# Performance work log

Hardware: AMD Instinct MI355X
Metric: run time of the kernel (lower is better)

The kernel has to match this reference:

```python
import jax, jax.numpy as jnp
import numpy as np

B = 1024      # batch
HG = 28       # grid side (28x28 image -> graph)
N = HG * HG   # 784 nodes per sample
K = 70        # node_sampled (relaxed categorical classes)
GCN_OUT = 48
H_DIM = 400
Z = 70
IMG = 784
TEMP = 0.5


def _grid_edges():
    idx = np.arange(N).reshape(HG, HG)
    src = np.concatenate([idx[:, :-1].ravel(), idx[:, 1:].ravel(), idx[:-1, :].ravel(), idx[1:, :].ravel()])
    dst = np.concatenate([idx[:, 1:].ravel(), idx[:, :-1].ravel(), idx[1:, :].ravel(), idx[:-1, :].ravel()])
    loop = np.arange(N)
    return (np.concatenate([src, loop]).astype(np.int32),
            np.concatenate([dst, loop]).astype(np.int32))


def _lin(key, fi, fo):
    kw, kb = jax.random.split(key)
    s = 1.0 / np.sqrt(fi)
    return (jax.random.uniform(kw, (fi, fo), jnp.float32, -s, s),
            jax.random.uniform(kb, (fo,), jnp.float32, -s, s))


def setup_inputs() -> dict:
    key = jax.random.key(0)
    ks = jax.random.split(key, 16)
    src, dst = _grid_edges()
    u = jax.random.uniform(ks[2], (B, N, K), jnp.float32, 1e-6, 1.0 - 1e-6)
    inp = {
        'nodes': jax.random.normal(ks[0], (B, N, 2), jnp.float32),
        'logits': jax.random.normal(ks[1], (B, N, K), jnp.float32),
        'gumbel': -jnp.log(-jnp.log(u)),
        'eps': jax.random.normal(ks[3], (B, Z), jnp.float32),
    }
    inp['W1'], inp['b1'] = _lin(ks[4], 2, 16)
    inp['W2'], inp['b2'] = _lin(ks[5], 16, 32)
    inp['W3'], inp['b3'] = _lin(ks[6], 32, GCN_OUT)
    inp['We1'], inp['be1'] = _lin(ks[7], K * GCN_OUT, H_DIM)
    inp['We2'], inp['be2'] = _lin(ks[8], H_DIM, H_DIM)
    inp['Wmu'], inp['bmu'] = _lin(ks[9], H_DIM, Z)
    inp['Wvar'], inp['bvar'] = _lin(ks[10], H_DIM, Z)
    inp['Wd1'], inp['bd1'] = _lin(ks[11], Z, H_DIM)
    inp['Wd2'], inp['bd2'] = _lin(ks[12], H_DIM, IMG)
    inp['edge_src'] = jnp.asarray(src)
    inp['edge_dst'] = jnp.asarray(dst)
    return inp


def reference(nodes, logits, gumbel, eps,
              W1, b1, W2, b2, W3, b3,
              We1, be1, We2, be2,
              Wmu, bmu, Wvar, bvar,
              Wd1, bd1, Wd2, bd2,
              edge_src, edge_dst):
    # symmetric GCN normalization with self loops (already in edge list)
    deg = jnp.zeros((N,), nodes.dtype).at[edge_dst].add(1.0)
    dinv = jax.lax.rsqrt(deg)
    norm = dinv[edge_src] * dinv[edge_dst]  # [E]

    def gcn(h, W, b):
        h = h @ W                                   # [B,N,Fout]
        msg = h[:, edge_src] * norm[None, :, None]  # gather + scale, [B,E,Fout]
        return jnp.zeros_like(h).at[:, edge_dst].add(msg) + b

    h = jax.nn.relu(gcn(nodes, W1, b1))
    h = jax.nn.relu(gcn(h, W2, b2))
    h = jax.nn.relu(gcn(h, W3, b3))            # [B,N,48]

    # RelaxedOneHotCategorical(temp=0.5).rsample() == gumbel-softmax
    sample = jax.nn.softmax((logits + gumbel) / TEMP, axis=-1)  # [B,N,K]
    g = jnp.einsum('bnk,bnf->bkf', sample, h).reshape(h.shape[0], K * GCN_OUT)

    # encoder MLP + reparameterize
    e = jax.nn.relu(g @ We1 + be1)
    e = jax.nn.relu(e @ We2 + be2)
    mu = e @ Wmu + bmu
    var = jax.nn.softplus(e @ Wvar + bvar)
    z = mu + eps * jnp.sqrt(var + 1e-10)

    # decoder
    d = jax.nn.relu(z @ Wd1 + bd1)
    x_rec = jax.nn.sigmoid(d @ Wd2 + bd2)      # [B,784]
    return x_rec
```

## Files before the change

kernel.cpp:

```cpp
#include <hip/hip_runtime.h>
#include <hip/hip_bf16.h>


#define BB 1024
#define HG 28
#define NN 784
#define KK 70
#define F3 48
#define HD 400
#define ZD 70
#define IMGD 784

typedef __hip_bfloat16 bf16;
typedef __attribute__((ext_vector_type(8))) short s8v;
typedef __attribute__((ext_vector_type(4))) float f32x4;

__device__ __forceinline__ float dinv_ij(int i, int j){
  int deg = 1 + (i>0) + (i<HG-1) + (j>0) + (j<HG-1);
  return rsqrtf((float)deg);
}

__device__ __forceinline__ unsigned pk2(float a, float b){
  union { bf16 h; unsigned short u; } ua, ub;
  ua.h = __float2bfloat16(a); ub.h = __float2bfloat16(b);
  return ((unsigned)ub.u << 16) | ua.u;
}

__global__ __launch_bounds__(256, 2)
void gcn_fused(const float* __restrict__ nodes,
               const float* __restrict__ W1, const float* __restrict__ b1,
               const float* __restrict__ W2, const float* __restrict__ b2,
               const float* __restrict__ W3, const float* __restrict__ b3,
               bf16* __restrict__ h3){
  __shared__ __align__(16) char smem[73216];
  float* regA = (float*)smem;
  float* regB = (float*)(smem + 36288);
  float* wbuf = (float*)(smem + 64512);
  float* W1s = wbuf;          float* b1s = wbuf + 32;
  float* W2s = wbuf + 48;     float* b2s = wbuf + 560;
  float* W3s = wbuf + 592;    float* b3s = wbuf + 2128;

  int tid = threadIdx.x;
  if (tid < 32)  W1s[tid] = W1[tid];
  if (tid < 16)  b1s[tid] = b1[tid];
  for (int t = tid; t < 512;  t += 256) W2s[t] = W2[t];
  if (tid < 32)  b2s[tid] = b2[tid];
  for (int t = tid; t < 1536; t += 256) W3s[t] = W3[t];
  if (tid < 48)  b3s[tid] = b3[tid];

  int b = blockIdx.x >> 2, s = blockIdx.x & 3;
  int base3 = s*7;
  int base2 = base3 - 1;
  int base1 = base3 - 2;
  const float* nb = nodes + (size_t)b*NN*2;
  __syncthreads();

  {
    float* h1s = regA;
    for (int t = tid; t < 308; t += 256){
      int lr = t/28, j = t - lr*28;
      int r = base1 + lr;
      float o[16] __attribute__((aligned(16)));
      if (r < 0 || r >= HG){
        #pragma unroll
        for (int f=0; f<16; f++) o[f] = 0.f;
      } else {
        float dn = dinv_ij(r,j);
        float a0 = dn*nb[(r*HG+j)*2+0], a1 = dn*nb[(r*HG+j)*2+1];
        if (r > 0)   { float w=dinv_ij(r-1,j); a0 += w*nb[((r-1)*HG+j)*2]; a1 += w*nb[((r-1)*HG+j)*2+1]; }
        if (r < HG-1){ float w=dinv_ij(r+1,j); a0 += w*nb[((r+1)*HG+j)*2]; a1 += w*nb[((r+1)*HG+j)*2+1]; }
        if (j > 0)   { float w=dinv_ij(r,j-1); a0 += w*nb[(r*HG+j-1)*2];   a1 += w*nb[(r*HG+j-1)*2+1]; }
        if (j < HG-1){ float w=dinv_ij(r,j+1); a0 += w*nb[(r*HG+j+1)*2];   a1 += w*nb[(r*HG+j+1)*2+1]; }
        a0 *= dn; a1 *= dn;
        #pragma unroll
        for (int f=0; f<16; f++) o[f] = fmaxf(a0*W1s[f] + a1*W1s[16+f] + b1s[f], 0.f);
      }
      float* dst = h1s + t*20;
      #pragma unroll
      for (int q=0; q<4; q++) *(float4*)(dst + 4*q) = *(float4*)&o[4*q];
    }
  }
  __syncthreads();

  if (tid < 252){
    const float* h1s = regA;
    float* agg1 = regB;
    int lr = tid/28, j = tid - lr*28;
    int r = base2 + lr;
    float o[16] __attribute__((aligned(16)));
    if (r < 0 || r >= HG){
      #pragma unroll
      for (int f=0; f<16; f++) o[f] = 0.f;
    } else {
      int ln = (lr+1)*28 + j;
      float dn = dinv_ij(r,j);
      float wu = dinv_ij(r-1,j), wd = dinv_ij(r+1,j);
      float wl = (j>0)    ? dinv_ij(r,j-1) : 0.f;
      float wr = (j<HG-1) ? dinv_ij(r,j+1) : 0.f;
      const float* pc = h1s + ln*20;
      #pragma unroll
      for (int q=0; q<4; q++){
        float4 vc = *(const float4*)(pc + 4*q);
        float4 vu = *(const float4*)(pc - 28*20 + 4*q);
        float4 vd = *(const float4*)(pc + 28*20 + 4*q);
        float4 vl = *(const float4*)(pc - 20 + 4*q);
        float4 vr = *(const float4*)(pc + 20 + 4*q);
        o[4*q+0] = dn*(dn*vc.x + wu*vu.x + wd*vd.x + wl*vl.x + wr*vr.x);
        o[4*q+1] = dn*(dn*vc.y + wu*vu.y + wd*vd.y + wl*vl.y + wr*vr.y);
        o[4*q+2] = dn*(dn*vc.z + wu*vu.z + wd*vd.z + wl*vl.z + wr*vr.z);
        o[4*q+3] = dn*(dn*vc.w + wu*vu.w + wd*vd.w + wl*vl.w + wr*vr.w);
      }
    }
    float* dst = agg1 + tid*20;
    #pragma unroll
    for (int q=0; q<4; q++) *(float4*)(dst + 4*q) = *(float4*)&o[4*q];
  }
  __syncthreads();

  {
    const float* agg1 = regB;
    float* h2s = regA;
    int tx = tid & 7, ty = tid >> 3;
    float4 w2r[16];
    #pragma unroll
    for (int fi=0; fi<16; fi++) w2r[fi] = *(const float4*)&W2s[fi*32 + tx*4];
    float4 bb = *(const float4*)&b2s[tx*4];
    #pragma unroll
    for (int i=0; i<8; i++){
      int n = ty + 32*i;
      if (n < 252){
        float af[16] __attribute__((aligned(16)));
        const float* ap = agg1 + n*20;
        #pragma unroll
        for (int q=0; q<4; q++) *(float4*)&af[4*q] = *(const float4*)(ap + 4*q);
        float4 acc = bb;
        #pragma unroll
        for (int fi=0; fi<16; fi++){
          float a = af[fi];
          acc.x += a*w2r[fi].x; acc.y += a*w2r[fi].y;
          acc.z += a*w2r[fi].z; acc.w += a*w2r[fi].w;
        }
        acc.x = fmaxf(acc.x,0.f); acc.y = fmaxf(acc.y,0.f);
        acc.z = fmaxf(acc.z,0.f); acc.w = fmaxf(acc.w,0.f);
        *(float4*)&h2s[n*36 + tx*4] = acc;
      }
    }
  }
  __syncthreads();

  if (tid < 196){
    const float* h2s = regA;
    float* agg2 = regB;
    int lr = tid/28, j = tid - lr*28;
    int r = base3 + lr;
    int ln = (lr+1)*28 + j;
    float dn = dinv_ij(r,j);
    float wu = dinv_ij(r-1,j), wd = dinv_ij(r+1,j);
    float wl = (j>0)    ? dinv_ij(r,j-1) : 0.f;
    float wr = (j<HG-1) ? dinv_ij(r,j+1) : 0.f;
    const float* pc = h2s + ln*36;
    float* dst = agg2 + tid*36;
    #pragma unroll
    for (int q=0; q<8; q++){
      float4 vc = *(const float4*)(pc + 4*q);
      float4 vu = *(const float4*)(pc - 28*36 + 4*q);
      float4 vd = *(const float4*)(pc + 28*36 + 4*q);
      float4 vl = *(const float4*)(pc - 36 + 4*q);
      float4 vr = *(const float4*)(pc + 36 + 4*q);
      float4 o;
      o.x = dn*(dn*vc.x + wu*vu.x + wd*vd.x + wl*vl.x + wr*vr.x);
      o.y = dn*(dn*vc.y + wu*vu.y + wd*vd.y + wl*vl.y + wr*vr.y);
      o.z = dn*(dn*vc.z + wu*vu.z + wd*vd.z + wl*vl.z + wr*vr.z);
      o.w = dn*(dn*vc.w + wu*vu.w + wd*vd.w + wl*vl.w + wr*vr.w);
      *(float4*)(dst + 4*q) = o;
    }
  }
  __syncthreads();

  {
    bf16* h3buf = (bf16*)regA;
    if (tid < 252){
      const float* agg2 = regB;
      int tx = tid % 12, ty = tid / 12;
      float4 w3r[32];
      #pragma unroll
      for (int fi=0; fi<32; fi++) w3r[fi] = *(const float4*)&W3s[fi*48 + tx*4];
      float4 bb = *(const float4*)&b3s[tx*4];
      #pragma unroll
      for (int i=0; i<10; i++){
        int n = ty + 21*i;
        if (n < 196){
          float af[32] __attribute__((aligned(16)));
          const float* ap = agg2 + n*36;
          #pragma unroll
          for (int q=0; q<8; q++) *(float4*)&af[4*q] = *(const float4*)(ap + 4*q);
          float4 acc = bb;
          #pragma unroll
          for (int fi=0; fi<32; fi++){
            float a = af[fi];
            acc.x += a*w3r[fi].x; acc.y += a*w3r[fi].y;
            acc.z += a*w3r[fi].z; acc.w += a*w3r[fi].w;
          }
          uint2 pv;
          pv.x = pk2(fmaxf(acc.x,0.f), fmaxf(acc.y,0.f));
          pv.y = pk2(fmaxf(acc.z,0.f), fmaxf(acc.w,0.f));
          *(uint2*)((char*)h3buf + n*112 + tx*8) = pv;
        }
      }
    }
  }
  __syncthreads();

  {
    const char* h3buf = (const char*)regA;
    uint4* dst = (uint4*)(h3 + ((size_t)b*NN + base3*28)*F3);
    for (int t = tid; t < 1176; t += 256){
      int n = t/6, gq = t - n*6;
      dst[t] = *(const uint4*)(h3buf + n*112 + gq*16);
    }
  }
}

__global__ __launch_bounds__(256, 2)
void einsum_mfma_kernel(const float* __restrict__ logits, const float* __restrict__ gumbel,
                        const bf16* __restrict__ h3, float* __restrict__ g){
  __shared__ __align__(16) char smem[72256];
  float* samp = (float*)smem;
  short* stp  = (short*)smem;
  short* stlo = (short*)(smem + 21760);
  short* htp  = (short*)(smem + 43520);
  float* cred = (float*)(smem + 43520 + 13056);

  int b = blockIdx.x;
  int tid = threadIdx.x;
  int l = tid & 63, w = tid >> 6;

  f32x4 acc[5][3];
  #pragma unroll
  for (int mt=0; mt<5; mt++)
    #pragma unroll
    for (int bt=0; bt<3; bt++) acc[mt][bt] = (f32x4){0.f,0.f,0.f,0.f};

  for (int chunk = 0; chunk < 7; chunk++){
    int c0 = chunk*128;
    int nvalid = min(128, NN - c0);
    __syncthreads();

    {
      const float4* l4 = (const float4*)(logits + ((size_t)b*NN + c0)*KK);
      const float4* g4 = (const float4*)(gumbel + ((size_t)b*NN + c0)*KK);
      int lim = nvalid*KK/4;
      for (int t = tid; t < 2240; t += 256){
        if (t < lim){
          float4 lv = l4[t], gv = g4[t];
          float xs[4] = {2.f*(lv.x+gv.x), 2.f*(lv.y+gv.y), 2.f*(lv.z+gv.z), 2.f*(lv.w+gv.w)};
          int e = t*4;
          #pragma unroll
          for (int i2=0;i2<4;i2++){
            int n = (e+i2)/KK, k = (e+i2) - KK*n;
            samp[n*72 + k] = xs[i2];
          }
        }
      }
    }
    {
      int n = tid & 127, fh = tid >> 7;
      bool valid = n < nvalid;
      const uint2* src = (const uint2*)(h3 + ((size_t)b*NN + c0 + n)*F3 + fh*24);
      #pragma unroll
      for (int j=0; j<6; j++){
        uint2 v = valid ? src[j] : (uint2){0u,0u};
        int f0 = fh*24 + j*4;
        htp[(f0+0)*136 + n] = (short)(v.x & 0xFFFFu);
        htp[(f0+1)*136 + n] = (short)(v.x >> 16);
        htp[(f0+2)*136 + n] = (short)(v.y & 0xFFFFu);
        htp[(f0+3)*136 + n] = (short)(v.y >> 16);
      }
    }
    __syncthreads();

    int nl = tid >> 1, h = tid & 1;
    bool valid = nl < nvalid;
    float p[35];
    if (valid){
      float x[35], m = -1e30f;
      #pragma unroll
      for (int t=0; t<35; t++){ x[t] = samp[nl*72 + h*35 + t]; m = fmaxf(m, x[t]); }
      m = fmaxf(m, __shfl_xor(m, 1));
      float sum = 0.f;
      #pragma unroll
      for (int t=0; t<35; t++){ x[t] = __expf(x[t]-m); sum += x[t]; }
      sum += __shfl_xor(sum, 1);
      float r = 1.0f/sum;
      #pragma unroll
      for (int t=0; t<35; t++) p[t] = x[t]*r;
    } else {
      #pragma unroll
      for (int t=0; t<35; t++) p[t] = 0.f;
    }
    __syncthreads();

    #pragma unroll
    for (int t=0; t<35; t++){
      int k = h*35 + t;
      bf16 hi = __float2bfloat16(p[t]);
      float lo = p[t] - __bfloat162float(hi);
      *(bf16*)&stp[k*136 + nl]  = hi;
      *(bf16*)&stlo[k*136 + nl] = __float2bfloat16(lo);
    }
    __syncthreads();

    {
      int n0 = w*32 + (l>>4)*8;
      s8v bfr[3];
      #pragma unroll
      for (int bt=0; bt<3; bt++)
        bfr[bt] = *(const s8v*)&htp[(bt*16 + (l&15))*136 + n0];
      #pragma unroll
      for (int mt=0; mt<5; mt++){
        s8v ah = *(const s8v*)&stp[(mt*16 + (l&15))*136 + n0];
        s8v al = *(const s8v*)&stlo[(mt*16 + (l&15))*136 + n0];
        #pragma unroll
        for (int bt=0; bt<3; bt++){
          acc[mt][bt] = __builtin_amdgcn_mfma_f32_16x16x32_bf16(ah, bfr[bt], acc[mt][bt], 0, 0, 0);
          acc[mt][bt] = __builtin_amdgcn_mfma_f32_16x16x32_bf16(al, bfr[bt], acc[mt][bt], 0, 0, 0);
        }
      }
    }
  }

  __syncthreads();
  for (int rw = 0; rw < 4; rw++){
    if (w == rw){
      #pragma unroll
      for (int mt=0; mt<5; mt++)
        #pragma unroll
        for (int bt=0; bt<3; bt++)
          #pragma unroll
          for (int r=0; r<4; r++){
            int row = mt*16 + (l>>4)*4 + r;
            int col = bt*16 + (l&15);
            if (rw == 0) cred[row*49 + col] = acc[mt][bt][r];
            else         cred[row*49 + col] += acc[mt][bt][r];
          }
    }
    __syncthreads();
  }
  for (int t = tid; t < KK*F3; t += 256){
    int r = t / F3, c = t - r*F3;
    g[(size_t)b*(KK*F3) + t] = cred[r*49 + c];
  }
}

template<int ACT>
__global__ __launch_bounds__(256)
void dense_kernel(const float* __restrict__ A, const float* __restrict__ W,
                  const float* __restrict__ bias, float* __restrict__ out,
                  int M, int K, int Nn, int kChunk){
  __shared__ float As[16][65];
  __shared__ float Bs[16][64];
  int tx = threadIdx.x & 15, ty = threadIdx.x >> 4;
  int m0 = blockIdx.x*64, n0 = blockIdx.y*64;
  int ks = blockIdx.z * kChunk;
  int ke = min(K, ks + kChunk);
  int a_kk = threadIdx.x & 15, a_mm = threadIdx.x >> 4;
  int b_nn = threadIdx.x & 63, b_k0 = threadIdx.x >> 6;
  float ra[4], rb[4];
  float acc[4][4] = {};

  #pragma unroll
  for (int s=0; s<4; s++){
    int gk = ks + a_kk;
    ra[s] = (gk < ke) ? A[(size_t)(m0 + a_mm + s*16)*K + gk] : 0.f;
  }
  #pragma unroll
  for (int s=0; s<4; s++){
    int gk = ks + b_k0 + s*4, gn = n0 + b_nn;
    rb[s] = (gk < ke && gn < Nn) ? W[(size_t)gk*Nn + gn] : 0.f;
  }

  for (int k0 = ks; k0 < ke; k0 += 16){
    #pragma unroll
    for (int s=0; s<4; s++) As[a_kk][a_mm + s*16] = ra[s];
    #pragma unroll
    for (int s=0; s<4; s++) Bs[b_k0 + s*4][b_nn] = rb[s];
    __syncthreads();
    if (k0 + 16 < ke){
      #pragma unroll
      for (int s=0; s<4; s++){
        int gk = k0 + 16 + a_kk;
        ra[s] = (gk < ke) ? A[(size_t)(m0 + a_mm + s*16)*K + gk] : 0.f;
      }
      #pragma unroll
      for (int s=0; s<4; s++){
        int gk = k0 + 16 + b_k0 + s*4, gn = n0 + b_nn;
        rb[s] = (gk < ke && gn < Nn) ? W[(size_t)gk*Nn + gn] : 0.f;
      }
    }
    #pragma unroll
    for (int kk=0; kk<16; kk++){
      float a[4], bv[4];
      #pragma unroll
      for (int i2=0; i2<4; i2++) a[i2] = As[kk][ty*4+i2];
      #pragma unroll
      for (int j2=0; j2<4; j2++) bv[j2] = Bs[kk][tx*4+j2];
      #pragma unroll
      for (int i2=0; i2<4; i2++)
        #pragma unroll
        for (int j2=0; j2<4; j2++) acc[i2][j2] += a[i2]*bv[j2];
    }
    __syncthreads();
  }

  if (ACT == 2){
    float* po = out + (size_t)blockIdx.z*M*Nn;
    #pragma unroll
    for (int j2=0; j2<4; j2++){
      int gn = n0 + tx*4 + j2;
      if (gn < Nn){
        #pragma unroll
        for (int i2=0; i2<4; i2++)
          po[(size_t)(m0 + ty*4 + i2)*Nn + gn] = acc[i2][j2];
      }
    }
  } else {
    #pragma unroll
    for (int j2=0; j2<4; j2++){
      int gn = n0 + tx*4 + j2;
      if (gn < Nn){
        float bb = bias[gn];
        #pragma unroll
        for (int i2=0; i2<4; i2++){
          float v = acc[i2][j2] + bb;
          v = (ACT == 0) ? fmaxf(v, 0.f) : 1.0f/(1.0f + __expf(-v));
          out[(size_t)(m0 + ty*4 + i2)*Nn + gn] = v;
        }
      }
    }
  }
}

__global__ __launch_bounds__(256)
void reduce_bias_relu(const float* __restrict__ part, const float* __restrict__ bias,
                      float* __restrict__ out, int M, int Nn, int S){
  int idx = blockIdx.x*256 + threadIdx.x;
  if (idx >= M*Nn) return;
  int n = idx % Nn;
  float s = bias[n];
  for (int i=0; i<S; i++) s += part[(size_t)i*M*Nn + idx];
  out[idx] = fmaxf(s, 0.f);
}

__global__ __launch_bounds__(256)
void latent_kernel(const float* __restrict__ e2,
                   const float* __restrict__ Wmu, const float* __restrict__ bmu,
                   const float* __restrict__ Wvar, const float* __restrict__ bvar,
                   const float* __restrict__ eps, float* __restrict__ z){
  int idx = blockIdx.x*256 + threadIdx.x;
  int b = idx / ZD, zi = idx - b*ZD;
  const float* er = e2 + (size_t)b*HD;
  float amu = 0.f, avr = 0.f;
  for (int j=0; j<HD; j++){
    float e = er[j];
    amu += e*Wmu[j*ZD + zi];
    avr += e*Wvar[j*ZD + zi];
  }
  float mu = amu + bmu[zi];
  float va = avr + bvar[zi];
  float sp = fmaxf(va, 0.f) + log1pf(__expf(-fabsf(va)));
  z[idx] = mu + eps[idx]*sqrtf(sp + 1e-10f);
}

extern "C" void kernel_launch(void* const* d_in, const int* in_sizes, int n_in,
                              void* d_out, int out_size, void* d_ws, size_t ws_size,
                              hipStream_t stream){
  (void)in_sizes; (void)n_in; (void)out_size; (void)ws_size;
  const float* nodes  = (const float*)d_in[0];
  const float* logits = (const float*)d_in[1];
  const float* gumbel = (const float*)d_in[2];
  const float* eps    = (const float*)d_in[3];
  const float* W1 =(const float*)d_in[4],  *b1 =(const float*)d_in[5];
  const float* W2 =(const float*)d_in[6],  *b2 =(const float*)d_in[7];
  const float* W3 =(const float*)d_in[8],  *b3 =(const float*)d_in[9];
  const float* We1=(const float*)d_in[10], *be1=(const float*)d_in[11];
  const float* We2=(const float*)d_in[12], *be2=(const float*)d_in[13];
  const float* Wmu=(const float*)d_in[14], *bmu=(const float*)d_in[15];
  const float* Wvr=(const float*)d_in[16], *bvr=(const float*)d_in[17];
  const float* Wd1=(const float*)d_in[18], *bd1=(const float*)d_in[19];
  const float* Wd2=(const float*)d_in[20], *bd2=(const float*)d_in[21];

  char* ws = (char*)d_ws;
  bf16*  h3 = (bf16*)(ws);
  float* g  = (float*)(ws + 77070336);
  float* e1 = (float*)(ws + 90832896);
  float* e2 = (float*)(ws + 92471296);
  float* zb = (float*)(ws + 94109696);
  float* dd = (float*)(ws + 94396416);
  float* part = (float*)(ws);
  float* out = (float*)d_out;

  gcn_fused<<<4096, 256, 0, stream>>>(nodes, W1, b1, W2, b2, W3, b3, h3);
  einsum_mfma_kernel<<<1024, 256, 0, stream>>>(logits, gumbel, h3, g);
  dense_kernel<2><<<dim3(16, 7, 8), 256, 0, stream>>>(g, We1, nullptr, part, 1024, 3360, 400, 432);
  reduce_bias_relu<<<1600, 256, 0, stream>>>(part, be1, e1, 1024, 400, 8);
  dense_kernel<0><<<dim3(16, 7, 1), 256, 0, stream>>>(e1, We2, be2, e2, 1024, 400, 400, 400);
  latent_kernel<<<280, 256, 0, stream>>>(e2, Wmu, bmu, Wvr, bvr, eps, zb);
  dense_kernel<0><<<dim3(16, 7, 1), 256, 0, stream>>>(zb, Wd1, bd1, dd, 1024, 70, 400, 70);
  dense_kernel<1><<<dim3(16, 13, 1), 256, 0, stream>>>(dd, Wd2, bd2, out, 1024, 400, 784, 400);
}
```

Before: 420.4 us.

## Software-pipeline einsum kernel with register prefetch and split M/K wave partition

Rewrites the gumbel-softmax einsum kernel to work on 64-node chunks and prefetch the next chunk's logits, gumbel and h3 into registers while the MFMAs for the current chunk run. Waves are now split into two K-halves by two M-halves instead of four K-slices, so the cross-wave reduction has two steps. Softmax uses four threads per node, and the padded smem layout is replaced by a contiguous one that needs less shared memory. The intent is to hide global load latency and to cut shared memory use and barrier count. In exchange it raises register pressure and drops the launch-bounds occupancy hint.

```diff
diff --git a/kernel.cpp b/kernel.cpp
--- a/kernel.cpp
+++ b/kernel.cpp
@@ -24,6 +24,10 @@
   union { bf16 h; unsigned short u; } ua, ub;
   ua.h = __float2bfloat16(a); ub.h = __float2bfloat16(b);
   return ((unsigned)ub.u << 16) | ua.u;
+}
+
+__device__ __forceinline__ short bfbits(float v){
+  union { bf16 h; short s; } u; u.h = __float2bfloat16(v); return u.s;
 }
 
 __global__ __launch_bounds__(256, 2)
@@ -221,134 +225,172 @@
   }
 }
 
-__global__ __launch_bounds__(256, 2)
+__global__ __launch_bounds__(256)
 void einsum_mfma_kernel(const float* __restrict__ logits, const float* __restrict__ gumbel,
                         const bf16* __restrict__ h3, float* __restrict__ g){
-  __shared__ __align__(16) char smem[72256];
+  __shared__ __align__(16) char smem[47872];
   float* samp = (float*)smem;
-  short* stp  = (short*)smem;
-  short* stlo = (short*)(smem + 21760);
-  short* htp  = (short*)(smem + 43520);
-  float* cred = (float*)(smem + 43520 + 13056);
+  short* stp  = (short*)(smem + 17920);
+  short* stlo = (short*)(smem + 29440);
+  short* htp  = (short*)(smem + 40960);
+  float* cred = (float*)smem;
 
   int b = blockIdx.x;
   int tid = threadIdx.x;
   int l = tid & 63, w = tid >> 6;
-
-  f32x4 acc[5][3];
+  int ks = w >> 1, mh = w & 1;
+  int mtoff = mh ? 3 : 0, mtcnt = mh ? 2 : 3;
+  int nl = tid >> 2, q = tid & 3;
+  int st = (q < 2) ? q*18 : 36 + (q-2)*17;
+  int cnt = (q < 2) ? 18 : 17;
+
+  f32x4 acc[3][3];
   #pragma unroll
-  for (int mt=0; mt<5; mt++)
+  for (int mt=0; mt<3; mt++)
     #pragma unroll
     for (int bt=0; bt<3; bt++) acc[mt][bt] = (f32x4){0.f,0.f,0.f,0.f};
 
-  for (int chunk = 0; chunk < 7; chunk++){
-    int c0 = chunk*128;
-    int nvalid = min(128, NN - c0);
+  float4 xs[5];
+  uint4 hv[2];
+
+  auto do_loads = [&](int c){
+    int c0 = c*64;
+    int nv = (c == 12) ? 16 : 64;
+    int lim4 = nv*70/4, limh = nv*6;
+    const float4* l4 = (const float4*)(logits + ((size_t)b*NN + c0)*KK);
+    const float4* g4 = (const float4*)(gumbel + ((size_t)b*NN + c0)*KK);
+    #pragma unroll
+    for (int s=0; s<5; s++){
+      int t = tid + s*256;
+      if (t < lim4){
+        float4 lv = l4[t], gv = g4[t];
+        xs[s] = (float4){2.f*(lv.x+gv.x), 2.f*(lv.y+gv.y), 2.f*(lv.z+gv.z), 2.f*(lv.w+gv.w)};
+      } else xs[s] = (float4){0.f,0.f,0.f,0.f};
+    }
+    const uint4* h4 = (const uint4*)(h3 + ((size_t)b*NN + c0)*F3);
+    #pragma unroll
+    for (int s=0; s<2; s++){
+      int t = tid + s*256;
+      hv[s] = (t < limh) ? h4[t] : (uint4){0u,0u,0u,0u};
+    }
+  };
+
+  auto write_samp = [&](){
+    #pragma unroll
+    for (int s=0; s<5; s++){
+      int t = tid + s*256;
+      if (t < 1120) ((float4*)samp)[t] = xs[s];
+    }
+  };
+
+  auto softmax_writes = [&](int c){
+    int nv = (c == 12) ? 16 : 64;
+    float p[18];
+    if (nl < nv){
+      float x[18];
+      float m = -1e30f;
+      #pragma unroll
+      for (int i=0; i<18; i++) if (i < cnt){ x[i] = samp[nl*70 + st + i]; m = fmaxf(m, x[i]); }
+      m = fmaxf(m, __shfl_xor(m, 1));
+      m = fmaxf(m, __shfl_xor(m, 2));
+      float sum = 0.f;
+      #pragma unroll
+      for (int i=0; i<18; i++) if (i < cnt){ x[i] = __expf(x[i]-m); sum += x[i]; }
+      sum += __shfl_xor(sum, 1);
+      sum += __shfl_xor(sum, 2);
+      float r = 1.0f/sum;
+      #pragma unroll
+      for (int i=0; i<18; i++) p[i] = x[i]*r;
+    } else {
+      #pragma unroll
+      for (int i=0; i<18; i++) p[i] = 0.f;
+    }
+    #pragma unroll
+    for (int i=0; i<18; i++) if (i < cnt){
+      int k = st + i;
+      short hi = bfbits(p[i]);
+      union { short s; bf16 h; } uh; uh.s = hi;
+      float lo = p[i] - __bfloat162float(uh.h);
+      stp[k*72 + nl]  = hi;
+      stlo[k*72 + nl] = bfbits(lo);
+    }
+    #pragma unroll
+    for (int s=0; s<2; s++){
+      int t = tid + s*256;
+      if (t < 384){
+        int n = t/6, j = t - n*6, f0 = j*8;
+        unsigned vv[4] = {hv[s].x, hv[s].y, hv[s].z, hv[s].w};
+        #pragma unroll
+        for (int i2=0; i2<4; i2++){
+          htp[(f0+2*i2  )*72 + n] = (short)(vv[i2] & 0xFFFFu);
+          htp[(f0+2*i2+1)*72 + n] = (short)(vv[i2] >> 16);
+        }
+      }
+    }
+  };
+
+  auto do_mfma = [&](){
+    int n0 = ks*32 + (l>>4)*8;
+    #pragma unroll
+    for (int bt=0; bt<3; bt++){
+      s8v bfr = *(const s8v*)&htp[(bt*16 + (l&15))*72 + n0];
+      #pragma unroll
+      for (int mt=0; mt<3; mt++) if (mt < mtcnt){
+        int row = (mtoff + mt)*16 + (l&15);
+        s8v ah = *(const s8v*)&stp[row*72 + n0];
+        s8v al = *(const s8v*)&stlo[row*72 + n0];
+        acc[mt][bt] = __builtin_amdgcn_mfma_f32_16x16x32_bf16(ah, bfr, acc[mt][bt], 0, 0, 0);
+        acc[mt][bt] = __builtin_amdgcn_mfma_f32_16x16x32_bf16(al, bfr, acc[mt][bt], 0, 0, 0);
+      }
+    }
+  };
+
+  do_loads(0);
+  write_samp();
+  __syncthreads();
+  softmax_writes(0);
+  __syncthreads();
+
+  for (int c = 0; c < 13; c++){
+    if (c < 12) do_loads(c+1);
+    do_mfma();
+    if (c < 12) write_samp();
     __syncthreads();
-
-    {
-      const float4* l4 = (const float4*)(logits + ((size_t)b*NN + c0)*KK);
-      const float4* g4 = (const float4*)(gumbel + ((size_t)b*NN + c0)*KK);
-      int lim = nvalid*KK/4;
-      for (int t = tid; t < 2240; t += 256){
-        if (t < lim){
-          float4 lv = l4[t], gv = g4[t];
-          float xs[4] = {2.f*(lv.x+gv.x), 2.f*(lv.y+gv.y), 2.f*(lv.z+gv.z), 2.f*(lv.w+gv.w)};
-          int e = t*4;
-          #pragma unroll
-          for (int i2=0;i2<4;i2++){
-            int n = (e+i2)/KK, k = (e+i2) - KK*n;
-            samp[n*72 + k] = xs[i2];
-          }
+    if (c < 12){
+      softmax_writes(c+1);
+      __syncthreads();
+    }
+  }
+
+  if (ks == 0){
+    #pragma unroll
+    for (int mt=0; mt<3; mt++) if (mt < mtcnt)
+      #pragma unroll
+      for (int bt=0; bt<3; bt++)
+        #pragma unroll
+        for (int r=0; r<4; r++){
+          int row = (mtoff+mt)*16 + (l>>4)*4 + r;
+          int col = bt*16 + (l&15);
+          cred[row*49 + col] = acc[mt][bt][r];
         }
-      }
-    }
-    {
-      int n = tid & 127, fh = tid >> 7;
-      bool valid = n < nvalid;
-      const uint2* src = (const uint2*)(h3 + ((size_t)b*NN + c0 + n)*F3 + fh*24);
-      #pragma unroll
-      for (int j=0; j<6; j++){
-        uint2 v = valid ? src[j] : (uint2){0u,0u};
-        int f0 = fh*24 + j*4;
-        htp[(f0+0)*136 + n] = (short)(v.x & 0xFFFFu);
-        htp[(f0+1)*136 + n] = (short)(v.x >> 16);
-        htp[(f0+2)*136 + n] = (short)(v.y & 0xFFFFu);
-        htp[(f0+3)*136 + n] = (short)(v.y >> 16);
-      }
-    }
-    __syncthreads();
-
-    int nl = tid >> 1, h = tid & 1;
-    bool valid = nl < nvalid;
-    float p[35];
-    if (valid){
-      float x[35], m = -1e30f;
-      #pragma unroll
-      for (int t=0; t<35; t++){ x[t] = samp[nl*72 + h*35 + t]; m = fmaxf(m, x[t]); }
-      m = fmaxf(m, __shfl_xor(m, 1));
-      float sum = 0.f;
-      #pragma unroll
-      for (int t=0; t<35; t++){ x[t] = __expf(x[t]-m); sum += x[t]; }
-      sum += __shfl_xor(sum, 1);
-      float r = 1.0f/sum;
-      #pragma unroll
-      for (int t=0; t<35; t++) p[t] = x[t]*r;
-    } else {
-      #pragma unroll
-      for (int t=0; t<35; t++) p[t] = 0.f;
-    }
-    __syncthreads();
-
-    #pragma unroll
-    for (int t=0; t<35; t++){
-      int k = h*35 + t;
-      bf16 hi = __float2bfloat16(p[t]);
-      float lo = p[t] - __bfloat162float(hi);
-      *(bf16*)&stp[k*136 + nl]  = hi;
-      *(bf16*)&stlo[k*136 + nl] = __float2bfloat16(lo);
-    }
-    __syncthreads();
-
-    {
-      int n0 = w*32 + (l>>4)*8;
-      s8v bfr[3];
+  }
+  __syncthreads();
+  if (ks == 1){
+    #pragma unroll
+    for (int mt=0; mt<3; mt++) if (mt < mtcnt)
       #pragma unroll
       for (int bt=0; bt<3; bt++)
-        bfr[bt] = *(const s8v*)&htp[(bt*16 + (l&15))*136 + n0];
-      #pragma unroll
-      for (int mt=0; mt<5; mt++){
-        s8v ah = *(const s8v*)&stp[(mt*16 + (l&15))*136 + n0];
-        s8v al = *(const s8v*)&stlo[(mt*16 + (l&15))*136 + n0];
-        #pragma unroll
-        for (int bt=0; bt<3; bt++){
-          acc[mt][bt] = __builtin_amdgcn_mfma_f32_16x16x32_bf16(ah, bfr[bt], acc[mt][bt], 0, 0, 0);
-          acc[mt][bt] = __builtin_amdgcn_mfma_f32_16x16x32_bf16(al, bfr[bt], acc[mt][bt], 0, 0, 0);
+        #pragma unroll
+        for (int r=0; r<4; r++){
+          int row = (mtoff+mt)*16 + (l>>4)*4 + r;
+          int col = bt*16 + (l&15);
+          cred[row*49 + col] += acc[mt][bt][r];
         }
-      }
-    }
-  }
-
-  __syncthreads();
-  for (int rw = 0; rw < 4; rw++){
-    if (w == rw){
-      #pragma unroll
-      for (int mt=0; mt<5; mt++)
-        #pragma unroll
-        for (int bt=0; bt<3; bt++)
-          #pragma unroll
-          for (int r=0; r<4; r++){
-            int row = mt*16 + (l>>4)*4 + r;
-            int col = bt*16 + (l&15);
-            if (rw == 0) cred[row*49 + col] = acc[mt][bt][r];
-            else         cred[row*49 + col] += acc[mt][bt][r];
-          }
-    }
-    __syncthreads();
-  }
+  }
+  __syncthreads();
   for (int t = tid; t < KK*F3; t += 256){
-    int r = t / F3, c = t - r*F3;
-    g[(size_t)b*(KK*F3) + t] = cred[r*49 + c];
+    int r = t / F3, c2 = t - r*F3;
+    g[(size_t)b*(KK*F3) + t] = cred[r*49 + c2];
   }
 }
 
```

Result: no change. 419.2 us (-0.3%).
